# Kernel tuning notes

Hardware: AMD Instinct MI355X
Metric: run time of the kernel (lower is better)

Reference implementation:

```python
import jax, jax.numpy as jnp
import numpy as np

silu = jax.nn.silu

B, N, E, H, T, L, A = 8, 20000, 40000, 128, 64, 4, 4


def setup_inputs() -> dict:
    key = jax.random.key(0)
    ks = jax.random.split(key, 20)
    s = 0.05
    w = lambda k, shape: jax.random.normal(k, shape, jnp.float32) * s
    return {
        "x": jax.random.normal(ks[0], (B, N, 3), jnp.float32),
        "t": jax.random.uniform(ks[1], (B,), jnp.float32) * 1000.0,
        "atom_types": jax.random.randint(ks[2], (N,), 0, A),
        "bond_indices": jax.random.randint(ks[3], (E, 2), 0, N),
        "emb_table": w(ks[4], (A, H)),
        "W_t1": w(ks[5], (T, H)), "b_t1": jnp.zeros((H,), jnp.float32),
        "W_t2": w(ks[6], (H, H)), "b_t2": jnp.zeros((H,), jnp.float32),
        "W_node": w(ks[7], (H, H)), "b_node": jnp.zeros((H,), jnp.float32),
        "Wm1": w(ks[8], (L, 2 * H + 1, H)), "bm1": jnp.zeros((L, H), jnp.float32),
        "Wm2": w(ks[9], (L, H, H)), "bm2": jnp.zeros((L, H), jnp.float32),
        "Wn1": w(ks[10], (L, 2 * H, H)), "bn1": jnp.zeros((L, H), jnp.float32),
        "Wn2": w(ks[11], (L, H, H)), "bn2": jnp.zeros((L, H), jnp.float32),
        "Wc1": w(ks[12], (L, H, H)), "bc1": jnp.zeros((L, H), jnp.float32),
        "Wc2": w(ks[13], (L, H, 1)) * 0.001,  # xavier gain=0.001 final coord layer
        "W_o1": w(ks[14], (H, H)), "b_o1": jnp.zeros((H,), jnp.float32),
        "W_o2": w(ks[15], (H, 3)), "b_o2": jnp.zeros((3,), jnp.float32),
    }


def reference(x, t, atom_types, bond_indices, emb_table,
              W_t1, b_t1, W_t2, b_t2, W_node, b_node,
              Wm1, bm1, Wm2, bm2, Wn1, bn1, Wn2, bn2, Wc1, bc1, Wc2,
              W_o1, b_o1, W_o2, b_o2):
    n_atoms = x.shape[1]
    src = bond_indices[:, 0]
    dst = bond_indices[:, 1]

    # sinusoidal time embedding -> time MLP
    half = W_t1.shape[0] // 2
    freq = jnp.exp(jnp.arange(half, dtype=jnp.float32) * (-np.log(10000.0) / (half - 1)))
    te = t[:, None] * freq[None, :]
    te = jnp.concatenate([jnp.sin(te), jnp.cos(te)], axis=-1)  # [B, T]
    t_emb = silu(te @ W_t1 + b_t1) @ W_t2 + b_t2  # [B, H]

    # node init: embedding -> linear -> + time emb
    h0 = emb_table[atom_types] @ W_node + b_node  # [N, H]
    h = h0[None, :, :] + t_emb[:, None, :]  # [B, N, H]

    # degree counts (src+dst incidence), clamped to >=1
    ones = jnp.ones((src.shape[0],), jnp.float32)
    counts = jnp.zeros((n_atoms,), jnp.float32).at[dst].add(ones).at[src].add(ones)
    counts = jnp.maximum(counts, 1.0)

    x_orig = x
    n_layers = Wm1.shape[0]
    for l in range(n_layers):
        h_src = h[:, src, :]
        h_dst = h[:, dst, :]
        coord_diff = x[:, dst, :] - x[:, src, :]  # [B, E, 3]
        dist = jnp.sqrt(jnp.sum(coord_diff * coord_diff, axis=-1, keepdims=True))
        msg_in = jnp.concatenate([h_src, h_dst, dist], axis=-1)  # [B, E, 2H+1]
        m = silu(msg_in @ Wm1[l] + bm1[l])
        m = silu(m @ Wm2[l] + bm2[l])  # [B, E, H]

        agg = jnp.zeros_like(h).at[:, dst, :].add(m).at[:, src, :].add(m)
        h_in = jnp.concatenate([h, agg], axis=-1)
        h = h + silu(h_in @ Wn1[l] + bn1[l]) @ Wn2[l] + bn2[l]

        cw = silu(m @ Wc1[l] + bc1[l]) @ Wc2[l]  # [B, E, 1]
        cdn = coord_diff / (dist + 1e-8)
        upd = cdn * cw
        coord_update = jnp.zeros_like(x).at[:, dst, :].add(upd).at[:, src, :].add(-upd)
        x = x + coord_update / counts[None, :, None]

    coord_change = x - x_orig
    noise_from_h = silu(h @ W_o1 + b_o1) @ W_o2 + b_o2
    return coord_change + noise_from_h
```

## Files before the change

kernel.cpp:

```cpp
#include <hip/hip_runtime.h>
#include <math.h>

#define B_ 8
#define N_ 20000
#define E_ 40000
#define H_ 128
#define L_ 4
#define A_ 4
#define MRS 136
#define EPB 64
#define NPB 64

#define WFENCE __asm__ __volatile__("" ::: "memory")

typedef _Float16 f16x8 __attribute__((ext_vector_type(8)));
typedef _Float16 f16x4v __attribute__((ext_vector_type(4)));
typedef float f32x4 __attribute__((ext_vector_type(4)));

__device__ __forceinline__ float silu_f(float x) {
    return x * __builtin_amdgcn_rcpf(1.f + __expf(-x));
}


__global__ void k_zero(int* __restrict__ deg, int* __restrict__ cursor) {
    int i = blockIdx.x * 256 + threadIdx.x;
    if (i < N_) { deg[i] = 0; cursor[i] = 0; }
}

__global__ void k_deg(const int* __restrict__ bond, int* __restrict__ deg) {
    int e = blockIdx.x * 256 + threadIdx.x;
    if (e < E_) {
        atomicAdd(&deg[bond[2 * e]], 1);
        atomicAdd(&deg[bond[2 * e + 1]], 1);
    }
}

__global__ void k_scan(const int* __restrict__ deg, int* __restrict__ indptr) {
    __shared__ int sums[1024];
    const int CH = (N_ + 1023) / 1024;
    int t = threadIdx.x;
    int s0 = t * CH;
    int s1 = min(s0 + CH, N_);
    int s = 0;
    for (int i = s0; i < s1; ++i) s += deg[i];
    sums[t] = s;
    __syncthreads();
    for (int off = 1; off < 1024; off <<= 1) {
        int v = (t >= off) ? sums[t - off] : 0;
        __syncthreads();
        sums[t] += v;
        __syncthreads();
    }
    int base = (t > 0) ? sums[t - 1] : 0;
    int run = base;
    for (int i = s0; i < s1; ++i) { indptr[i] = run; run += deg[i]; }
    if (s1 == N_ && s0 < N_) indptr[N_] = run;
}

__global__ void k_fill(const int* __restrict__ bond, const int* __restrict__ indptr,
                       int* __restrict__ cursor, int* __restrict__ adj) {
    int e = blockIdx.x * 256 + threadIdx.x;
    if (e < E_) {
        int s = bond[2 * e], d = bond[2 * e + 1];
        int ps = indptr[s] + atomicAdd(&cursor[s], 1);
        adj[ps] = (e << 1);
        int pd = indptr[d] + atomicAdd(&cursor[d], 1);
        adj[pd] = (e << 1) | 1;
    }
}

__global__ void k_wprepL(const float* __restrict__ W, _Float16* __restrict__ Wf,
                         int K, int wstride) {
    int l = blockIdx.y;
    const float* Wl = W + (size_t)l * wstride;
    _Float16* Wfl = Wf + (size_t)l * K * 128;
    int idx = blockIdx.x * 256 + threadIdx.x;
    if (idx >= K * 128) return;
    int j = idx & 7, lane = (idx >> 3) & 63, nt = (idx >> 9) & 7, kt = idx >> 12;
    int k = kt * 32 + (lane >> 4) * 8 + j;
    int n = nt * 16 + (lane & 15);
    Wfl[idx] = (_Float16)Wl[k * 128 + n];
}

__global__ void k_temb(const float* __restrict__ tv,
                       const float* __restrict__ W1, const float* __restrict__ b1,
                       const float* __restrict__ W2, const float* __restrict__ b2,
                       float* __restrict__ t_emb) {
    __shared__ float te[64];
    __shared__ float h1[128];
    int b = blockIdx.x;
    int tid = threadIdx.x;
    float tval = tv[b];
    if (tid < 32) {
        float fr = __expf((float)tid * (-logf(10000.f) / 31.f));
        float a = tval * fr;
        te[tid] = sinf(a);
        te[tid + 32] = cosf(a);
    }
    __syncthreads();
    float acc = b1[tid];
    for (int k = 0; k < 64; ++k) acc += te[k] * W1[k * 128 + tid];
    h1[tid] = silu_f(acc);
    __syncthreads();
    float acc2 = b2[tid];
    for (int k = 0; k < 128; ++k) acc2 += h1[k] * W2[k * 128 + tid];
    t_emb[b * 128 + tid] = acc2;
}

__global__ void k_embproj(const float* __restrict__ emb, const float* __restrict__ W,
                          const float* __restrict__ bias, float* __restrict__ outp) {
    int tid = threadIdx.x;
    int a = tid >> 7, j = tid & 127;
    float acc = bias[j];
    for (int k = 0; k < 128; ++k) acc += emb[a * 128 + k] * W[k * 128 + j];
    outp[a * 128 + j] = acc;
}

__global__ void k_hinit(const int* __restrict__ at, const float* __restrict__ embp,
                        const float* __restrict__ temb, float* __restrict__ h,
                        _Float16* __restrict__ h16) {
    size_t idx4 = (size_t)blockIdx.x * 256 + threadIdx.x;
    size_t e0 = idx4 * 4;
    int j = (int)(e0 % H_);
    size_t bn = e0 / H_;
    int n = (int)(bn % N_);
    int b = (int)(bn / N_);
    int a = at[n];
    float4 ep = *(const float4*)(embp + a * H_ + j);
    float4 tv = *(const float4*)(temb + b * H_ + j);
    float4 r = make_float4(ep.x + tv.x, ep.y + tv.y, ep.z + tv.z, ep.w + tv.w);
    ((float4*)h)[idx4] = r;
    f16x4v o;
    o[0] = (_Float16)r.x; o[1] = (_Float16)r.y; o[2] = (_Float16)r.z; o[3] = (_Float16)r.w;
    *(f16x4v*)(h16 + e0) = o;
}

__global__ void k_xcopy(const float* __restrict__ x, float* __restrict__ xb) {
    int i = blockIdx.x * 256 + threadIdx.x;
    xb[i] = x[i];
}

template <int RS, int KT>
__device__ __forceinline__ void mfma_gemm(const _Float16* Asw, const _Float16* __restrict__ Wf,
                                          f32x4 (&acc)[8], int ml, int quad, int lane) {
    #pragma unroll
    for (int kt = 0; kt < KT; ++kt) {
        f16x8 a = *(const f16x8*)(Asw + ml * RS + kt * 32 + quad * 8);
        #pragma unroll
        for (int nt = 0; nt < 8; ++nt) {
            f16x8 b = *(const f16x8*)(Wf + (((kt * 8 + nt) * 64 + lane) * 8));
            acc[nt] = __builtin_amdgcn_mfma_f32_16x16x32_f16(a, b, acc[nt], 0, 0, 0);
        }
    }
}

template <int RS, int KT>
__device__ __forceinline__ void mfma_gemm2(const _Float16* Asw, const _Float16* __restrict__ Wf,
                                           f32x4 (&acc)[2][8], int ml, int quad, int lane) {
    #pragma unroll
    for (int kt = 0; kt < KT; ++kt) {
        f16x8 a0 = *(const f16x8*)(Asw + ml * RS + kt * 32 + quad * 8);
        f16x8 a1 = *(const f16x8*)(Asw + (16 + ml) * RS + kt * 32 + quad * 8);
        #pragma unroll
        for (int nt = 0; nt < 8; ++nt) {
            f16x8 b = *(const f16x8*)(Wf + (((kt * 8 + nt) * 64 + lane) * 8));
            acc[0][nt] = __builtin_amdgcn_mfma_f32_16x16x32_f16(a0, b, acc[0][nt], 0, 0, 0);
            acc[1][nt] = __builtin_amdgcn_mfma_f32_16x16x32_f16(a1, b, acc[1][nt], 0, 0, 0);
        }
    }
}

__device__ __forceinline__ void load_row(f16x8 (&v)[4], const _Float16* mp) {
    #pragma unroll
    for (int j = 0; j < 4; ++j) v[j] = *(const f16x8*)(mp + j * 8);
}
__device__ __forceinline__ void acc_row(float (&ag)[4][8], const f16x8 (&v)[4]) {
    #pragma unroll
    for (int j = 0; j < 4; ++j)
        #pragma unroll
        for (int i = 0; i < 8; ++i) ag[j][i] += (float)v[j][i];
}


__global__ __launch_bounds__(128, 3) void k_edge_mfma(
    const _Float16* __restrict__ h16, const float* __restrict__ xcur,
    const int* __restrict__ bond,
    const float* __restrict__ Wm1, const float* __restrict__ bm1,
    const _Float16* __restrict__ Wm1f,
    const float* __restrict__ bm2, const _Float16* __restrict__ Wm2f,
    const float* __restrict__ bc1, const _Float16* __restrict__ Wc1f,
    const float* __restrict__ Wc2,
    _Float16* __restrict__ m16, float* __restrict__ cw_out) {
    __shared__ _Float16 As[EPB * MRS];
    __shared__ float ds_s[EPB];
    int tid = threadIdx.x;
    int b = blockIdx.x & 7;
    int e0 = (blockIdx.x >> 3) * EPB;
    size_t be0 = (size_t)b * E_ + e0;

    int el = tid >> 1, q = tid & 1;
    int2 sd = ((const int2*)bond)[e0 + el];
    int s = sd.x, d = sd.y;

    const _Float16* hs = h16 + ((size_t)b * N_ + s) * H_ + q * 64;
    const _Float16* hd = h16 + ((size_t)b * N_ + d) * H_ + q * 64;
    f16x8 ps[8], pd[8];
    #pragma unroll
    for (int j = 0; j < 8; ++j) ps[j] = *(const f16x8*)(hs + j * 8);
    #pragma unroll
    for (int j = 0; j < 8; ++j) pd[j] = *(const f16x8*)(hd + j * 8);
    if (q == 0) {
        const float* xs = xcur + ((size_t)b * N_ + s) * 3;
        const float* xd = xcur + ((size_t)b * N_ + d) * 3;
        float dx = xd[0] - xs[0], dy = xd[1] - xs[1], dz = xd[2] - xs[2];
        ds_s[el] = sqrtf(dx * dx + dy * dy + dz * dz);
    }
    {
        _Float16* ap = As + el * MRS + q * 64;
        #pragma unroll
        for (int j = 0; j < 8; ++j) *(f16x8*)(ap + j * 8) = ps[j];
    }
    WFENCE;

    int lane = tid & 63, w = tid >> 6;
    int ml = lane & 15, quad = lane >> 4;
    _Float16* Asw = As + w * 32 * MRS;
    const float* wd = Wm1 + 256 * H_;

    f32x4 acc[2][8];
    #pragma unroll
    for (int nt = 0; nt < 8; ++nt) {
        int col = nt * 16 + ml;
        float bb = bm1[col];
        float ww = wd[col];
        #pragma unroll
        for (int rt = 0; rt < 2; ++rt)
            #pragma unroll
            for (int r = 0; r < 4; ++r)
                acc[rt][nt][r] = bb + ds_s[w * 32 + rt * 16 + quad * 4 + r] * ww;
    }
    mfma_gemm2<MRS, 4>(Asw, Wm1f, acc, ml, quad, lane);
    WFENCE;
    {
        _Float16* ap = As + el * MRS + q * 64;
        #pragma unroll
        for (int j = 0; j < 8; ++j) *(f16x8*)(ap + j * 8) = pd[j];
    }
    WFENCE;
    mfma_gemm2<MRS, 4>(Asw, Wm1f + 4 * 8 * 64 * 8, acc, ml, quad, lane);
    WFENCE;
    #pragma unroll
    for (int rt = 0; rt < 2; ++rt)
        #pragma unroll
        for (int nt = 0; nt < 8; ++nt)
            #pragma unroll
            for (int r = 0; r < 4; ++r)
                Asw[(rt * 16 + quad * 4 + r) * MRS + nt * 16 + ml] = (_Float16)silu_f(acc[rt][nt][r]);
    WFENCE;

    #pragma unroll
    for (int nt = 0; nt < 8; ++nt) {
        float bb = bm2[nt * 16 + ml];
        #pragma unroll
        for (int rt = 0; rt < 2; ++rt)
            #pragma unroll
            for (int r = 0; r < 4; ++r) acc[rt][nt][r] = bb;
    }
    mfma_gemm2<MRS, 4>(Asw, Wm2f, acc, ml, quad, lane);
    WFENCE;
    #pragma unroll
    for (int rt = 0; rt < 2; ++rt)
        #pragma unroll
        for (int nt = 0; nt < 8; ++nt)
            #pragma unroll
            for (int r = 0; r < 4; ++r)
                Asw[(rt * 16 + quad * 4 + r) * MRS + nt * 16 + ml] = (_Float16)silu_f(acc[rt][nt][r]);
    WFENCE;
    #pragma unroll
    for (int j = 0; j < 8; ++j)
        *(f16x8*)(m16 + (be0 + el) * H_ + q * 64 + j * 8) =
            *(const f16x8*)(As + el * MRS + q * 64 + j * 8);

    #pragma unroll
    for (int nt = 0; nt < 8; ++nt) {
        float bb = bc1[nt * 16 + ml];
        #pragma unroll
        for (int rt = 0; rt < 2; ++rt)
            #pragma unroll
            for (int r = 0; r < 4; ++r) acc[rt][nt][r] = bb;
    }
    mfma_gemm2<MRS, 4>(Asw, Wc1f, acc, ml, quad, lane);
    float part[2][4] = {{0.f, 0.f, 0.f, 0.f}, {0.f, 0.f, 0.f, 0.f}};
    #pragma unroll
    for (int nt = 0; nt < 8; ++nt) {
        float wv = Wc2[nt * 16 + ml];
        #pragma unroll
        for (int rt = 0; rt < 2; ++rt)
            #pragma unroll
            for (int r = 0; r < 4; ++r) part[rt][r] += silu_f(acc[rt][nt][r]) * wv;
    }
    #pragma unroll
    for (int off = 1; off < 16; off <<= 1)
        #pragma unroll
        for (int rt = 0; rt < 2; ++rt)
            #pragma unroll
            for (int r = 0; r < 4; ++r) part[rt][r] += __shfl_xor(part[rt][r], off, 64);
    if (ml == 0) {
        #pragma unroll
        for (int rt = 0; rt < 2; ++rt)
            #pragma unroll
            for (int r = 0; r < 4; ++r)
                cw_out[be0 + w * 32 + rt * 16 + quad * 4 + r] = part[rt][r];
    }
}

__global__ void k_coord(const float* __restrict__ xcur, float* __restrict__ xnext,
                        const float* __restrict__ cw, const int* __restrict__ bond,
                        const int* __restrict__ indptr, const int* __restrict__ adj) {
    int idx = blockIdx.x * 256 + threadIdx.x;
    int b = idx / N_;
    int n = idx - b * N_;
    const float* xb = xcur + (size_t)b * N_ * 3;
    int p0 = indptr[n], p1 = indptr[n + 1];
    float ax = 0.f, ay = 0.f, az = 0.f;
    for (int p = p0; p < p1; ++p) {
        int a = adj[p];
        int e = a >> 1;
        float sgn = (a & 1) ? 1.f : -1.f;
        int s = bond[2 * e], d = bond[2 * e + 1];
        float dx = xb[d * 3 + 0] - xb[s * 3 + 0];
        float dy = xb[d * 3 + 1] - xb[s * 3 + 1];
        float dz = xb[d * 3 + 2] - xb[s * 3 + 2];
        float dist = sqrtf(dx * dx + dy * dy + dz * dz);
        float w = cw[(size_t)b * E_ + e] * sgn * __builtin_amdgcn_rcpf(dist + 1e-8f);
        ax += dx * w; ay += dy * w; az += dz * w;
    }
    float rcnt = __builtin_amdgcn_rcpf((float)max(p1 - p0, 1));
    xnext[(size_t)idx * 3 + 0] = xb[n * 3 + 0] + ax * rcnt;
    xnext[(size_t)idx * 3 + 1] = xb[n * 3 + 1] + ay * rcnt;
    xnext[(size_t)idx * 3 + 2] = xb[n * 3 + 2] + az * rcnt;
}

__global__ __launch_bounds__(256, 4) void k_node_mfma(
    float* __restrict__ h, _Float16* __restrict__ h16,
    const _Float16* __restrict__ m16,
    const int* __restrict__ indptr, const int* __restrict__ adj,
    const float* __restrict__ bn1, const _Float16* __restrict__ Wn1f,
    const float* __restrict__ bn2, const _Float16* __restrict__ Wn2f) {
    __shared__ _Float16 As[NPB * MRS];
    int tid = threadIdx.x;
    int el = tid >> 2, q = tid & 3;
    int be = blockIdx.x * NPB + el;
    int b = be / N_, n = be - b * N_;
    {
        const _Float16* hr = h16 + (size_t)be * H_;
        #pragma unroll
        for (int j = 0; j < 4; ++j)
            *(f16x8*)(As + el * MRS + q * 32 + j * 8) = *(const f16x8*)(hr + q * 32 + j * 8);
    }
    int p0 = indptr[n], p1 = indptr[n + 1];
    int d0 = p1 - p0;
    const _Float16* mbb = m16 + (size_t)b * E_ * H_;
    int ea = (d0 > 0) ? (adj[p0] >> 1) : 0;
    int eb = (d0 > 1) ? (adj[p0 + 1] >> 1) : ea;
    f16x8 va[4], vb[4];
    load_row(va, mbb + (size_t)ea * H_ + q * 32);
    load_row(vb, mbb + (size_t)eb * H_ + q * 32);
    WFENCE;

    int lane = tid & 63, w = tid >> 6;
    int ml = lane & 15, quad = lane >> 4;
    _Float16* Asw = As + w * 16 * MRS;
    size_t be0 = (size_t)blockIdx.x * NPB;

    f32x4 acc[8];
    #pragma unroll
    for (int nt = 0; nt < 8; ++nt) {
        float bb = bn1[nt * 16 + ml];
        #pragma unroll
        for (int r = 0; r < 4; ++r) acc[nt][r] = bb;
    }
    mfma_gemm<MRS, 4>(Asw, Wn1f, acc, ml, quad, lane);
    WFENCE;
    {
        float ag[4][8];
        #pragma unroll
        for (int j = 0; j < 4; ++j)
            #pragma unroll
            for (int i = 0; i < 8; ++i) ag[j][i] = 0.f;
        if (d0 > 0) acc_row(ag, va);
        if (d0 > 1) acc_row(ag, vb);
        int p = p0 + 2;
        while (p + 2 <= p1) {
            int e1 = adj[p] >> 1, e2 = adj[p + 1] >> 1;
            f16x8 w1[4], w2[4];
            load_row(w1, mbb + (size_t)e1 * H_ + q * 32);
            load_row(w2, mbb + (size_t)e2 * H_ + q * 32);
            acc_row(ag, w1);
            acc_row(ag, w2);
            p += 2;
        }
        if (p < p1) {
            int e1 = adj[p] >> 1;
            f16x8 w1[4];
            load_row(w1, mbb + (size_t)e1 * H_ + q * 32);
            acc_row(ag, w1);
        }
        #pragma unroll
        for (int j = 0; j < 4; ++j) {
            f16x8 o;
            #pragma unroll
            for (int i = 0; i < 8; ++i) o[i] = (_Float16)ag[j][i];
            *(f16x8*)(As + el * MRS + q * 32 + j * 8) = o;
        }
    }
    WFENCE;
    mfma_gemm<MRS, 4>(Asw, Wn1f + 4 * 8 * 64 * 8, acc, ml, quad, lane);
    WFENCE;
    #pragma unroll
    for (int nt = 0; nt < 8; ++nt)
        #pragma unroll
        for (int r = 0; r < 4; ++r)
            Asw[(quad * 4 + r) * MRS + nt * 16 + ml] = (_Float16)silu_f(acc[nt][r]);
    WFENCE;
    f32x4 acc2[8];
    #pragma unroll
    for (int nt = 0; nt < 8; ++nt) {
        float bb = bn2[nt * 16 + ml];
        #pragma unroll
        for (int r = 0; r < 4; ++r) acc2[nt][r] = bb;
    }
    mfma_gemm<MRS, 4>(Asw, Wn2f, acc2, ml, quad, lane);
    #pragma unroll
    for (int nt = 0; nt < 8; ++nt)
        #pragma unroll
        for (int r = 0; r < 4; ++r) {
            int row = w * 16 + quad * 4 + r;
            size_t g = (size_t)(be0 + row) * H_ + nt * 16 + ml;
            float v = h[g] + acc2[nt][r];
            h[g] = v;
            h16[g] = (_Float16)v;
        }
}

__global__ __launch_bounds__(256, 4) void k_out_mfma(
    const _Float16* __restrict__ h16, const float* __restrict__ xfin, const float* __restrict__ xorig,
    const _Float16* __restrict__ Wo1f, const float* __restrict__ bo1,
    const float* __restrict__ Wo2, const float* __restrict__ bo2,
    float* __restrict__ out) {
    __shared__ _Float16 As[64 * MRS];
    __shared__ float red[64 * 48];
    int tid = threadIdx.x;
    int el = tid >> 2, q = tid & 3;
    size_t be = (size_t)blockIdx.x * 64 + el;
    {
        const _Float16* hr = h16 + be * H_;
        #pragma unroll
        for (int j = 0; j < 4; ++j)
            *(f16x8*)(As + el * MRS + q * 32 + j * 8) = *(const f16x8*)(hr + q * 32 + j * 8);
    }
    WFENCE;

    int lane = tid & 63, w = tid >> 6;
    int ml = lane & 15, quad = lane >> 4;
    _Float16* Asw = As + w * 16 * MRS;

    f32x4 acc[8];
    #pragma unroll
    for (int nt = 0; nt < 8; ++nt) {
        float bb = bo1[nt * 16 + ml];
        #pragma unroll
        for (int r = 0; r < 4; ++r) acc[nt][r] = bb;
    }
    mfma_gemm<MRS, 4>(Asw, Wo1f, acc, ml, quad, lane);
    #pragma unroll
    for (int r = 0; r < 4; ++r) {
        float p0 = 0.f, p1 = 0.f, p2 = 0.f;
        #pragma unroll
        for (int nt = 0; nt < 8; ++nt) {
            float u = silu_f(acc[nt][r]);
            int col = nt * 16 + ml;
            p0 += u * Wo2[col * 3 + 0];
            p1 += u * Wo2[col * 3 + 1];
            p2 += u * Wo2[col * 3 + 2];
        }
        int row = w * 16 + quad * 4 + r;
        red[row * 48 + ml * 3 + 0] = p0;
        red[row * 48 + ml * 3 + 1] = p1;
        red[row * 48 + ml * 3 + 2] = p2;
    }
    __syncthreads();
    if (tid < 192) {
        int row = tid / 3, jj = tid - row * 3;
        float s = 0.f;
        #pragma unroll
        for (int cc = 0; cc < 16; ++cc) s += red[row * 48 + cc * 3 + jj];
        size_t grow = (size_t)blockIdx.x * 64 + row;
        out[grow * 3 + jj] = s + bo2[jj] + xfin[grow * 3 + jj] - xorig[grow * 3 + jj];
    }
}


extern "C" void kernel_launch(void* const* d_in, const int* in_sizes, int n_in,
                              void* d_out, int out_size, void* d_ws, size_t ws_size,
                              hipStream_t stream) {
    const float* x = (const float*)d_in[0];
    const float* t = (const float*)d_in[1];
    const int* atom_types = (const int*)d_in[2];
    const int* bond = (const int*)d_in[3];
    const float* emb_table = (const float*)d_in[4];
    const float* W_t1 = (const float*)d_in[5];
    const float* b_t1 = (const float*)d_in[6];
    const float* W_t2 = (const float*)d_in[7];
    const float* b_t2 = (const float*)d_in[8];
    const float* W_node = (const float*)d_in[9];
    const float* b_node = (const float*)d_in[10];
    const float* Wm1 = (const float*)d_in[11];
    const float* bm1 = (const float*)d_in[12];
    const float* Wm2 = (const float*)d_in[13];
    const float* bm2 = (const float*)d_in[14];
    const float* Wn1 = (const float*)d_in[15];
    const float* bn1 = (const float*)d_in[16];
    const float* Wn2 = (const float*)d_in[17];
    const float* bn2 = (const float*)d_in[18];
    const float* Wc1 = (const float*)d_in[19];
    const float* bc1 = (const float*)d_in[20];
    const float* Wc2 = (const float*)d_in[21];
    const float* W_o1 = (const float*)d_in[22];
    const float* b_o1 = (const float*)d_in[23];
    const float* W_o2 = (const float*)d_in[24];
    const float* b_o2 = (const float*)d_in[25];
    float* out = (float*)d_out;

    char* p = (char*)d_ws;
    auto alloc = [&](size_t bytes) -> void* {
        void* r = (void*)p;
        p += (bytes + 255) & ~(size_t)255;
        return r;
    };
    float* t_emb = (float*)alloc((size_t)B_ * H_ * 4);
    float* emb_proj = (float*)alloc((size_t)A_ * H_ * 4);
    int* deg = (int*)alloc((size_t)N_ * 4);
    int* indptr = (int*)alloc((size_t)(N_ + 1) * 4);
    int* cursor = (int*)alloc((size_t)N_ * 4);
    int* adj = (int*)alloc((size_t)2 * E_ * 4);
    float* xb0 = (float*)alloc((size_t)B_ * N_ * 3 * 4);
    float* xb1 = (float*)alloc((size_t)B_ * N_ * 3 * 4);
    float* cw = (float*)alloc((size_t)B_ * E_ * 4);
    float* h = (float*)alloc((size_t)B_ * N_ * H_ * 4);
    _Float16* h16 = (_Float16*)alloc((size_t)B_ * N_ * H_ * 2);
    _Float16* m16 = (_Float16*)alloc((size_t)B_ * E_ * H_ * 2);
    _Float16* Wm1f = (_Float16*)alloc((size_t)L_ * 256 * H_ * 2);
    _Float16* Wm2f = (_Float16*)alloc((size_t)L_ * H_ * H_ * 2);
    _Float16* Wc1f = (_Float16*)alloc((size_t)L_ * H_ * H_ * 2);
    _Float16* Wn1f = (_Float16*)alloc((size_t)L_ * 256 * H_ * 2);
    _Float16* Wn2f = (_Float16*)alloc((size_t)L_ * H_ * H_ * 2);
    _Float16* Wo1f = (_Float16*)alloc((size_t)H_ * H_ * 2);

    k_zero<<<(N_ + 255) / 256, 256, 0, stream>>>(deg, cursor);
    k_deg<<<(E_ + 255) / 256, 256, 0, stream>>>(bond, deg);
    k_scan<<<1, 1024, 0, stream>>>(deg, indptr);
    k_fill<<<(E_ + 255) / 256, 256, 0, stream>>>(bond, indptr, cursor, adj);
    k_temb<<<B_, 128, 0, stream>>>(t, W_t1, b_t1, W_t2, b_t2, t_emb);
    k_embproj<<<1, 512, 0, stream>>>(emb_table, W_node, b_node, emb_proj);
    k_hinit<<<(B_ * N_ * H_ / 4) / 256, 256, 0, stream>>>(atom_types, emb_proj, t_emb, h, h16);
    k_xcopy<<<(B_ * N_ * 3) / 256, 256, 0, stream>>>(x, xb0);
    k_wprepL<<<dim3(128, L_), 256, 0, stream>>>(Wm1, Wm1f, 256, 257 * H_);
    k_wprepL<<<dim3(64, L_), 256, 0, stream>>>(Wm2, Wm2f, 128, H_ * H_);
    k_wprepL<<<dim3(64, L_), 256, 0, stream>>>(Wc1, Wc1f, 128, H_ * H_);
    k_wprepL<<<dim3(128, L_), 256, 0, stream>>>(Wn1, Wn1f, 256, 2 * H_ * H_);
    k_wprepL<<<dim3(64, L_), 256, 0, stream>>>(Wn2, Wn2f, 128, H_ * H_);
    k_wprepL<<<dim3(64, 1), 256, 0, stream>>>(W_o1, Wo1f, 128, H_ * H_);

    float* xc = xb0;
    float* xn = xb1;
    for (int l = 0; l < L_; ++l) {
        k_edge_mfma<<<(B_ * E_) / EPB, 128, 0, stream>>>(
            h16, xc, bond,
            Wm1 + (size_t)l * 257 * H_, bm1 + l * H_, Wm1f + (size_t)l * 256 * H_,
            bm2 + l * H_, Wm2f + (size_t)l * H_ * H_,
            bc1 + l * H_, Wc1f + (size_t)l * H_ * H_,
            Wc2 + (size_t)l * H_, m16, cw);
        k_coord<<<(B_ * N_) / 256, 256, 0, stream>>>(xc, xn, cw, bond, indptr, adj);
        k_node_mfma<<<(B_ * N_) / NPB, 256, 0, stream>>>(
            h, h16, m16, indptr, adj,
            bn1 + l * H_, Wn1f + (size_t)l * 256 * H_,
            bn2 + l * H_, Wn2f + (size_t)l * H_ * H_);
        float* tmp = xc; xc = xn; xn = tmp;
    }
    k_out_mfma<<<(B_ * N_) / 64, 256, 0, stream>>>(h16, xc, x, Wo1f, b_o1, W_o2, b_o2, out);
}
```

Measured before the change: 1.004 ms.

## Fuse coordinate scatter into edge kernel with atomics, replace CSR gather

The edge kernel now computes each edge's normalized coordinate update and scatters it with float atomics into a per-node accumulation buffer. This replaces the cw buffer and the CSR-based k_coord gather, which re-read bonds and coordinates. A light k_xupd kernel applies the update scaled by 1/degree and re-zeros the buffer for the next layer. It trades a gather pass for atomic contention and makes floating-point summation order nondeterministic.

```diff
diff --git a/kernel.cpp b/kernel.cpp
--- a/kernel.cpp
+++ b/kernel.cpp
@@ -25,6 +25,11 @@
 __global__ void k_zero(int* __restrict__ deg, int* __restrict__ cursor) {
     int i = blockIdx.x * 256 + threadIdx.x;
     if (i < N_) { deg[i] = 0; cursor[i] = 0; }
+}
+
+__global__ void k_zero3(float* __restrict__ cupd) {
+    int i = blockIdx.x * 256 + threadIdx.x;
+    cupd[i] = 0.f;
 }
 
 __global__ void k_deg(const int* __restrict__ bond, int* __restrict__ deg) {
@@ -190,9 +195,11 @@
     const float* __restrict__ bm2, const _Float16* __restrict__ Wm2f,
     const float* __restrict__ bc1, const _Float16* __restrict__ Wc1f,
     const float* __restrict__ Wc2,
-    _Float16* __restrict__ m16, float* __restrict__ cw_out) {
+    _Float16* __restrict__ m16, float* __restrict__ cupd) {
     __shared__ _Float16 As[EPB * MRS];
     __shared__ float ds_s[EPB];
+    __shared__ float dx_s[EPB], dy_s[EPB], dz_s[EPB];
+    __shared__ int s_s[EPB], d_s[EPB];
     int tid = threadIdx.x;
     int b = blockIdx.x & 7;
     int e0 = (blockIdx.x >> 3) * EPB;
@@ -214,6 +221,8 @@
         const float* xd = xcur + ((size_t)b * N_ + d) * 3;
         float dx = xd[0] - xs[0], dy = xd[1] - xs[1], dz = xd[2] - xs[2];
         ds_s[el] = sqrtf(dx * dx + dy * dy + dz * dz);
+        dx_s[el] = dx; dy_s[el] = dy; dz_s[el] = dz;
+        s_s[el] = s; d_s[el] = d;
     }
     {
         _Float16* ap = As + el * MRS + q * 64;
@@ -305,40 +314,34 @@
         for (int rt = 0; rt < 2; ++rt)
             #pragma unroll
             for (int r = 0; r < 4; ++r) part[rt][r] += __shfl_xor(part[rt][r], off, 64);
-    if (ml == 0) {
+    if (ml < 2) {
+        float sgn = (ml == 0) ? 1.f : -1.f;
         #pragma unroll
         for (int rt = 0; rt < 2; ++rt)
             #pragma unroll
-            for (int r = 0; r < 4; ++r)
-                cw_out[be0 + w * 32 + rt * 16 + quad * 4 + r] = part[rt][r];
-    }
-}
-
-__global__ void k_coord(const float* __restrict__ xcur, float* __restrict__ xnext,
-                        const float* __restrict__ cw, const int* __restrict__ bond,
-                        const int* __restrict__ indptr, const int* __restrict__ adj) {
+            for (int r = 0; r < 4; ++r) {
+                int ee = w * 32 + rt * 16 + quad * 4 + r;
+                float wv = part[rt][r] * __builtin_amdgcn_rcpf(ds_s[ee] + 1e-8f) * sgn;
+                int node = (ml == 0) ? d_s[ee] : s_s[ee];
+                float* cp = cupd + ((size_t)b * N_ + node) * 3;
+                atomicAdd(cp + 0, dx_s[ee] * wv);
+                atomicAdd(cp + 1, dy_s[ee] * wv);
+                atomicAdd(cp + 2, dz_s[ee] * wv);
+            }
+    }
+}
+
+__global__ void k_xupd(const float* __restrict__ xcur, float* __restrict__ xnext,
+                       float* __restrict__ cupd, const int* __restrict__ deg) {
     int idx = blockIdx.x * 256 + threadIdx.x;
-    int b = idx / N_;
-    int n = idx - b * N_;
-    const float* xb = xcur + (size_t)b * N_ * 3;
-    int p0 = indptr[n], p1 = indptr[n + 1];
-    float ax = 0.f, ay = 0.f, az = 0.f;
-    for (int p = p0; p < p1; ++p) {
-        int a = adj[p];
-        int e = a >> 1;
-        float sgn = (a & 1) ? 1.f : -1.f;
-        int s = bond[2 * e], d = bond[2 * e + 1];
-        float dx = xb[d * 3 + 0] - xb[s * 3 + 0];
-        float dy = xb[d * 3 + 1] - xb[s * 3 + 1];
-        float dz = xb[d * 3 + 2] - xb[s * 3 + 2];
-        float dist = sqrtf(dx * dx + dy * dy + dz * dz);
-        float w = cw[(size_t)b * E_ + e] * sgn * __builtin_amdgcn_rcpf(dist + 1e-8f);
-        ax += dx * w; ay += dy * w; az += dz * w;
-    }
-    float rcnt = __builtin_amdgcn_rcpf((float)max(p1 - p0, 1));
-    xnext[(size_t)idx * 3 + 0] = xb[n * 3 + 0] + ax * rcnt;
-    xnext[(size_t)idx * 3 + 1] = xb[n * 3 + 1] + ay * rcnt;
-    xnext[(size_t)idx * 3 + 2] = xb[n * 3 + 2] + az * rcnt;
+    int n = idx % N_;
+    float rcnt = __builtin_amdgcn_rcpf((float)max(deg[n], 1));
+    #pragma unroll
+    for (int j = 0; j < 3; ++j) {
+        size_t g = (size_t)idx * 3 + j;
+        xnext[g] = xcur[g] + cupd[g] * rcnt;
+        cupd[g] = 0.f;
+    }
 }
 
 __global__ __launch_bounds__(256, 4) void k_node_mfma(
@@ -546,7 +549,7 @@
     int* adj = (int*)alloc((size_t)2 * E_ * 4);
     float* xb0 = (float*)alloc((size_t)B_ * N_ * 3 * 4);
     float* xb1 = (float*)alloc((size_t)B_ * N_ * 3 * 4);
-    float* cw = (float*)alloc((size_t)B_ * E_ * 4);
+    float* cupd = (float*)alloc((size_t)B_ * N_ * 3 * 4);
     float* h = (float*)alloc((size_t)B_ * N_ * H_ * 4);
     _Float16* h16 = (_Float16*)alloc((size_t)B_ * N_ * H_ * 2);
     _Float16* m16 = (_Float16*)alloc((size_t)B_ * E_ * H_ * 2);
@@ -558,6 +561,7 @@
     _Float16* Wo1f = (_Float16*)alloc((size_t)H_ * H_ * 2);
 
     k_zero<<<(N_ + 255) / 256, 256, 0, stream>>>(deg, cursor);
+    k_zero3<<<(B_ * N_ * 3) / 256, 256, 0, stream>>>(cupd);
     k_deg<<<(E_ + 255) / 256, 256, 0, stream>>>(bond, deg);
     k_scan<<<1, 1024, 0, stream>>>(deg, indptr);
     k_fill<<<(E_ + 255) / 256, 256, 0, stream>>>(bond, indptr, cursor, adj);
@@ -580,8 +584,8 @@
             Wm1 + (size_t)l * 257 * H_, bm1 + l * H_, Wm1f + (size_t)l * 256 * H_,
             bm2 + l * H_, Wm2f + (size_t)l * H_ * H_,
             bc1 + l * H_, Wc1f + (size_t)l * H_ * H_,
-            Wc2 + (size_t)l * H_, m16, cw);
-        k_coord<<<(B_ * N_) / 256, 256, 0, stream>>>(xc, xn, cw, bond, indptr, adj);
+            Wc2 + (size_t)l * H_, m16, cupd);
+        k_xupd<<<(B_ * N_) / 256, 256, 0, stream>>>(xc, xn, cupd, deg);
         k_node_mfma<<<(B_ * N_) / NPB, 256, 0, stream>>>(
             h, h16, m16, indptr, adj,
             bn1 + l * H_, Wn1f + (size_t)l * 256 * H_,
```

Result: slower. 1.145 ms (+14.1%).
